# Performance work log

Hardware: AMD Instinct MI355X
Metric: run time of the kernel (lower is better)

Reference implementation:

```python
import jax, jax.numpy as jnp
import numpy as np

B, H, W, C, K = 32, 256, 256, 3, 32


def setup_inputs() -> dict:
    key = jax.random.key(0)
    k1, k2 = jax.random.split(key)
    images = jax.random.uniform(k1, (B, H, W, C), dtype=jnp.float32)
    palettes = jax.random.uniform(k2, (B, K, C), dtype=jnp.float32)
    temperature = jnp.ones((), dtype=jnp.float32)
    return {"images": images, "palettes": palettes, "temperature": temperature}


def reference(images, palettes, temperature):
    # distances: [b, h, w, k] = sum_c (img[b,h,w,c] - palette[b,k,c])^2
    diff = images[:, :, :, None, :] - palettes[:, None, None, :, :]
    distances = jnp.sum(diff * diff, axis=-1)
    # soft assignment (training path): softmax over palette entries
    weights = jax.nn.softmax(-distances / temperature, axis=-1)  # [b,h,w,k]
    # weighted combine: [b,h,w,c]
    return jnp.einsum('bhwk,bkc->bhwc', weights, palettes)
```

## Files before the change

kernel.cpp:

```cpp
#include <hip/hip_runtime.h>

#define LOG2E 1.44269504088896340736f

__device__ __forceinline__ float fast_exp2(float x) {
#if __has_builtin(__builtin_amdgcn_exp2f)
    return __builtin_amdgcn_exp2f(x);
#else
    return exp2f(x);
#endif
}

constexpr int BATCH = 32;
constexpr int CH = 3;
constexpr int KPAL = 32;
constexpr int PIX_PER_BATCH = 256 * 256;
constexpr int THREADS = 256;
constexpr int BLOCKS_PER_BATCH = PIX_PER_BATCH / THREADS;
constexpr int NBLOCKS = BATCH * BLOCKS_PER_BATCH;

struct F3 { float x, y, z; };

__global__ __launch_bounds__(THREADS, 8)
void palette_quant_kernel(const float* __restrict__ images,
                          const float* __restrict__ palettes,
                          const float* __restrict__ temp,
                          float* __restrict__ out)
{
    __shared__ float4 ab[KPAL];
    __shared__ float s_fs;

    const int batch = blockIdx.x >> 8;

    if (threadIdx.x < KPAL) {
        const float T = *temp;
        const float cinv = LOG2E / T;
        const float* p = palettes + (batch * KPAL + threadIdx.x) * CH;
        const float p0 = p[0], p1 = p[1], p2 = p[2];
        const float b = -(p0 * p0 + p1 * p1 + p2 * p2) * cinv;
        const float c2 = 2.0f * cinv;
        ab[threadIdx.x] = make_float4(p0 * c2, p1 * c2, p2 * c2, b);
        if (threadIdx.x == 0) s_fs = T * (0.5f / LOG2E);
    }
    __syncthreads();

    const long long pix  = (long long)blockIdx.x * THREADS + threadIdx.x;
    const long long base = pix * CH;

    const F3 v = *reinterpret_cast<const F3*>(images + base);
    const float x0 = v.x, x1 = v.y, x2 = v.z;

    float sum = 0.f, o0 = 0.f, o1 = 0.f, o2 = 0.f;

#pragma unroll
    for (int k = 0; k < KPAL; ++k) {
        const float4 a = ab[k];
        float s = fmaf(x0, a.x, a.w);
        s = fmaf(x1, a.y, s);
        s = fmaf(x2, a.z, s);
        const float w = fast_exp2(s);
        sum += w;
        o0 = fmaf(w, a.x, o0);
        o1 = fmaf(w, a.y, o1);
        o2 = fmaf(w, a.z, o2);
    }

    const float r = s_fs * __builtin_amdgcn_rcpf(sum);
    F3 o;
    o.x = o0 * r;
    o.y = o1 * r;
    o.z = o2 * r;
    *reinterpret_cast<F3*>(out + base) = o;
}

extern "C" void kernel_launch(void* const* d_in, const int* in_sizes, int n_in,
                              void* d_out, int out_size, void* d_ws, size_t ws_size,
                              hipStream_t stream) {
    const float* images   = (const float*)d_in[0];
    const float* palettes = (const float*)d_in[1];
    const float* temp     = (const float*)d_in[2];
    float* out            = (float*)d_out;

    palette_quant_kernel<<<dim3(NBLOCKS), dim3(THREADS), 0, stream>>>(
        images, palettes, temp, out);
}
```

Before: 87.67 us.

## Precompute palette coefficients in a separate kernel and use packed FP32 math for two pixels per thread

```diff
diff --git a/kernel.cpp b/kernel.cpp
--- a/kernel.cpp
+++ b/kernel.cpp
@@ -1,6 +1,8 @@
 #include <hip/hip_runtime.h>
 
 #define LOG2E 1.44269504088896340736f
+
+typedef float v2f __attribute__((ext_vector_type(2)));
 
 __device__ __forceinline__ float fast_exp2(float x) {
 #if __has_builtin(__builtin_amdgcn_exp2f)
@@ -13,63 +15,102 @@
 constexpr int BATCH = 32;
 constexpr int CH = 3;
 constexpr int KPAL = 32;
+constexpr int NPAIR = KPAL / 2;
 constexpr int PIX_PER_BATCH = 256 * 256;
 constexpr int THREADS = 256;
-constexpr int BLOCKS_PER_BATCH = PIX_PER_BATCH / THREADS;
+constexpr int PIX_PER_THREAD = 2;
+constexpr int BLOCKS_PER_BATCH = PIX_PER_BATCH / (THREADS * PIX_PER_THREAD);
 constexpr int NBLOCKS = BATCH * BLOCKS_PER_BATCH;
+constexpr int COEFF_PER_BATCH = NPAIR * 8;
 
-struct F3 { float x, y, z; };
 
-__global__ __launch_bounds__(THREADS, 8)
+__global__ void palette_coeff_kernel(const float* __restrict__ palettes,
+                                     const float* __restrict__ temp,
+                                     float* __restrict__ ws)
+{
+    const int t = blockIdx.x * blockDim.x + threadIdx.x;
+    if (t >= BATCH * NPAIR) return;
+    const int batch = t >> 4;
+    const int j = t & (NPAIR - 1);
+
+    const float T = *temp;
+    const float cinv = LOG2E / T;
+    const float c2 = 2.0f * cinv;
+
+    const float* p = palettes + batch * KPAL * CH + (2 * j) * CH;
+    const float e0 = p[0], e1 = p[1], e2 = p[2];
+    const float f0 = p[3], f1 = p[4], f2 = p[5];
+
+    float* w = ws + batch * COEFF_PER_BATCH + j * 8;
+    w[0] = e0 * c2;  w[1] = f0 * c2;
+    w[2] = e1 * c2;  w[3] = f1 * c2;
+    w[4] = e2 * c2;  w[5] = f2 * c2;
+    w[6] = -(e0 * e0 + e1 * e1 + e2 * e2) * cinv;
+    w[7] = -(f0 * f0 + f1 * f1 + f2 * f2) * cinv;
+}
+
+__global__ __launch_bounds__(THREADS, 4)
 void palette_quant_kernel(const float* __restrict__ images,
-                          const float* __restrict__ palettes,
+                          const float* __restrict__ coeffs,
                           const float* __restrict__ temp,
                           float* __restrict__ out)
 {
-    __shared__ float4 ab[KPAL];
-    __shared__ float s_fs;
+    const int batch = blockIdx.x >> 7;
+    const float* cb = coeffs + batch * COEFF_PER_BATCH;
 
-    const int batch = blockIdx.x >> 8;
+    const long long pp   = (long long)blockIdx.x * THREADS + threadIdx.x;
+    const long long base = pp * (PIX_PER_THREAD * CH);
 
-    if (threadIdx.x < KPAL) {
-        const float T = *temp;
-        const float cinv = LOG2E / T;
-        const float* p = palettes + (batch * KPAL + threadIdx.x) * CH;
-        const float p0 = p[0], p1 = p[1], p2 = p[2];
-        const float b = -(p0 * p0 + p1 * p1 + p2 * p2) * cinv;
-        const float c2 = 2.0f * cinv;
-        ab[threadIdx.x] = make_float4(p0 * c2, p1 * c2, p2 * c2, b);
-        if (threadIdx.x == 0) s_fs = T * (0.5f / LOG2E);
-    }
-    __syncthreads();
+    const v2f v0 = *reinterpret_cast<const v2f*>(images + base);
+    const v2f v1 = *reinterpret_cast<const v2f*>(images + base + 2);
+    const v2f v2_ = *reinterpret_cast<const v2f*>(images + base + 4);
 
-    const long long pix  = (long long)blockIdx.x * THREADS + threadIdx.x;
-    const long long base = pix * CH;
+    const v2f XA0 = {v0.x, v0.x}, XA1 = {v0.y, v0.y}, XA2 = {v1.x, v1.x};
+    const v2f XB0 = {v1.y, v1.y}, XB1 = {v2_.x, v2_.x}, XB2 = {v2_.y, v2_.y};
 
-    const F3 v = *reinterpret_cast<const F3*>(images + base);
-    const float x0 = v.x, x1 = v.y, x2 = v.z;
-
-    float sum = 0.f, o0 = 0.f, o1 = 0.f, o2 = 0.f;
+    v2f sumA = {0.f, 0.f}, oA0 = {0.f, 0.f}, oA1 = {0.f, 0.f}, oA2 = {0.f, 0.f};
+    v2f sumB = {0.f, 0.f}, oB0 = {0.f, 0.f}, oB1 = {0.f, 0.f}, oB2 = {0.f, 0.f};
 
 #pragma unroll
-    for (int k = 0; k < KPAL; ++k) {
-        const float4 a = ab[k];
-        float s = fmaf(x0, a.x, a.w);
-        s = fmaf(x1, a.y, s);
-        s = fmaf(x2, a.z, s);
-        const float w = fast_exp2(s);
-        sum += w;
-        o0 = fmaf(w, a.x, o0);
-        o1 = fmaf(w, a.y, o1);
-        o2 = fmaf(w, a.z, o2);
+    for (int j = 0; j < NPAIR; ++j) {
+        const v2f A0 = *reinterpret_cast<const v2f*>(cb + 8 * j + 0);
+        const v2f A1 = *reinterpret_cast<const v2f*>(cb + 8 * j + 2);
+        const v2f A2 = *reinterpret_cast<const v2f*>(cb + 8 * j + 4);
+        const v2f Bb = *reinterpret_cast<const v2f*>(cb + 8 * j + 6);
+        {
+            v2f s = __builtin_elementwise_fma(XA0, A0, Bb);
+            s = __builtin_elementwise_fma(XA1, A1, s);
+            s = __builtin_elementwise_fma(XA2, A2, s);
+            v2f w; w.x = fast_exp2(s.x); w.y = fast_exp2(s.y);
+            sumA += w;
+            oA0 = __builtin_elementwise_fma(w, A0, oA0);
+            oA1 = __builtin_elementwise_fma(w, A1, oA1);
+            oA2 = __builtin_elementwise_fma(w, A2, oA2);
+        }
+        {
+            v2f s = __builtin_elementwise_fma(XB0, A0, Bb);
+            s = __builtin_elementwise_fma(XB1, A1, s);
+            s = __builtin_elementwise_fma(XB2, A2, s);
+            v2f w; w.x = fast_exp2(s.x); w.y = fast_exp2(s.y);
+            sumB += w;
+            oB0 = __builtin_elementwise_fma(w, A0, oB0);
+            oB1 = __builtin_elementwise_fma(w, A1, oB1);
+            oB2 = __builtin_elementwise_fma(w, A2, oB2);
+        }
     }
 
-    const float r = s_fs * __builtin_amdgcn_rcpf(sum);
-    F3 o;
-    o.x = o0 * r;
-    o.y = o1 * r;
-    o.z = o2 * r;
-    *reinterpret_cast<F3*>(out + base) = o;
+    const float T = *temp;
+    const float fs = T * (0.5f / LOG2E);
+    const float rA = fs * __builtin_amdgcn_rcpf(sumA.x + sumA.y);
+    const float rB = fs * __builtin_amdgcn_rcpf(sumB.x + sumB.y);
+
+    const v2f w0 = {(oA0.x + oA0.y) * rA, (oA1.x + oA1.y) * rA};
+    const v2f w1 = {(oA2.x + oA2.y) * rA, (oB0.x + oB0.y) * rB};
+    const v2f w2 = {(oB1.x + oB1.y) * rB, (oB2.x + oB2.y) * rB};
+
+    *reinterpret_cast<v2f*>(out + base)     = w0;
+    *reinterpret_cast<v2f*>(out + base + 2) = w1;
+    *reinterpret_cast<v2f*>(out + base + 4) = w2;
 }
 
 extern "C" void kernel_launch(void* const* d_in, const int* in_sizes, int n_in,
@@ -79,7 +120,9 @@
     const float* palettes = (const float*)d_in[1];
     const float* temp     = (const float*)d_in[2];
     float* out            = (float*)d_out;
+    float* ws             = (float*)d_ws;
 
+    palette_coeff_kernel<<<dim3(2), dim3(256), 0, stream>>>(palettes, temp, ws);
     palette_quant_kernel<<<dim3(NBLOCKS), dim3(THREADS), 0, stream>>>(
-        images, palettes, temp, out);
+        images, ws, temp, out);
 }
```

New measurement: 88.28 us. Within noise of the previous version (+0.7%).
